# Optimization experiments

Measured on AMD Instinct MI355X. Metric: run time of the kernel, lower is better.

Reference implementation:

```python
import jax, jax.numpy as jnp
import numpy as np
import math

# ---- hyperparameters (from __init__) ----
S = 64.0
M = 0.45
EASY_MARGIN = False
ALPHA = 0.0
BETA = 0.0
EPS_OT = 0.1   # self.eps
NITER = 6      # self.niter
COS_M = math.cos(M)
SIN_M = math.sin(M)
TH = math.cos(math.pi - M)
MM = math.sin(math.pi - M) * M

# ---- shapes ----
B = 24
D_EMB = 512
N_CLASSES = 10000
C_CH = 256   # channels -> number of OT points per image
H = 14       # spatial -> point dim H*H = 196


def setup_inputs() -> dict:
    key = jax.random.key(0)
    k1, k2, k3, k4 = jax.random.split(key, 4)
    embeddings = jax.random.normal(k1, (B, D_EMB), dtype=jnp.float32)
    conv_features = jax.random.normal(k2, (B, C_CH, H, H), dtype=jnp.float32)
    label = jax.random.randint(k3, (B,), 0, 8)
    # nn.init.normal_(kernel, std=0.01)
    kernel = jax.random.normal(k4, (D_EMB, N_CLASSES), dtype=jnp.float32) * 0.01
    return {"embeddings": embeddings, "conv_features": conv_features,
            "kernel": kernel, "label": label, "epoch": 1}


def _cdist(x, y):
    # Euclidean pairwise distance via GEMM: x (n,d), y (m,d) -> (n,m)
    x2 = jnp.sum(x * x, axis=-1)[:, None]
    y2 = jnp.sum(y * y, axis=-1)[None, :]
    d2 = jnp.maximum(x2 + y2 - 2.0 * (x @ y.T), 0.0)
    return jnp.sqrt(d2 + 1e-12)


def _sinkhorn_dist(x, y):
    # Entropic OT distance <T, C> with uniform marginals, log-domain Sinkhorn.
    C = _cdist(x, y)                       # (n, m)
    n, m = C.shape
    log_mu = -jnp.log(jnp.float32(n))
    log_nu = -jnp.log(jnp.float32(m))
    f = jnp.zeros((n,), C.dtype)
    g = jnp.zeros((m,), C.dtype)
    for _ in range(NITER):  # fixed 6 iterations
        f = -EPS_OT * jax.nn.logsumexp((g[None, :] - C) / EPS_OT + log_nu, axis=1)
        g = -EPS_OT * jax.nn.logsumexp((f[:, None] - C) / EPS_OT + log_mu, axis=0)
    T = jnp.exp((f[:, None] + g[None, :] - C) / EPS_OT + log_mu + log_nu)
    return jnp.sum(T * C)


def reference(embeddings, conv_features, kernel, label, epoch):
    b = embeddings.shape[0]
    emb = embeddings / jnp.linalg.norm(embeddings, axis=1, keepdims=True)
    kn = kernel / jnp.linalg.norm(kernel, axis=0, keepdims=True)
    cos_theta = jnp.clip(emb @ kn, -1.0, 1.0)          # (B, n_classes)
    origin_cos = cos_theta

    rows = jnp.arange(b)
    tl = cos_theta[rows, label]                         # target logit (B,)
    sin_t = jnp.sqrt(jnp.maximum(1.0 - tl * tl, 0.0))
    ctm = tl * COS_M - sin_t * SIN_M
    if EASY_MARGIN:
        ftl = jnp.where(tl > 0.0, ctm, tl)
    else:
        ftl = jnp.where(tl > TH, ctm, tl - MM)
    cos_theta = cos_theta.at[rows, label].set(ftl)
    arcfaceloss = cos_theta * S

    # ---- triplet mining on embedding cosine similarities ----
    dists = emb @ emb.T                                 # (B, B) cosine sims
    eq = label[:, None] == label[None, :]               # (B, B) same-class mask
    # diff_low[a,p,n] = cos(a,n) - cos(a,p)
    diff = dists[:, None, :] - dists[:, :, None]        # (a, p, n)
    valid = eq[:, :, None] & (~eq)[:, None, :] & (diff > -ALPHA)
    n_cosine_pair = jnp.sum(valid)

    if epoch >= 0:
        feats = conv_features.reshape(b, conv_features.shape[1], -1)  # (B, C, H*H)
        # batched Sinkhorn distance for all (a,b) image pairs: (B, B)
        D = jax.vmap(lambda xa: jax.vmap(lambda xb: _sinkhorn_dist(xa, xb))(feats))(feats)
        dis = jnp.maximum(D[:, :, None] - D[:, None, :], -BETA)       # (a, p, n)
        hit = valid & (dis > 0.0)
        ot_pair = jnp.sum(hit)
        wass = jnp.sum(jnp.where(hit, dis, 0.0))
        wass_loss = jnp.where(wass > 0.0,
                              wass / jnp.maximum(ot_pair, 1).astype(wass.dtype),
                              jnp.zeros((), wass.dtype))
    else:
        ot_pair = jnp.zeros((), jnp.int32)
        wass_loss = jnp.zeros(())

    return (arcfaceloss, wass_loss, origin_cos * S, n_cosine_pair, ot_pair)
```

## Files before the change

kernel.cpp:

```cpp
#include <hip/hip_runtime.h>
#include <math.h>

#define B_SZ 24
#define D_EMBD 512
#define N_CLS 10000
#define CC 256
#define HH 196

#define S_SCALE 64.0f
#define COS_M 0.9004471023526769f
#define SIN_M 0.43496553411123023f
#define TH_C (-0.9004471023526769f)
#define MM_C 0.19573449035005357f
#define KSC 14.4269504088896f
#define C2E 0.0693147180559945f

typedef short bfrag8 __attribute__((ext_vector_type(8)));
typedef float facc4 __attribute__((ext_vector_type(4)));

#if __has_builtin(__builtin_amdgcn_exp2f)
#define EXP2F(x) __builtin_amdgcn_exp2f(x)
#else
#define EXP2F(x) exp2f(x)
#endif
#if __has_builtin(__builtin_amdgcn_logf)
#define LOG2F(x) __builtin_amdgcn_logf(x)
#else
#define LOG2F(x) __log2f(x)
#endif

__device__ inline unsigned short f2bf_rne(float x) {
    union { float f; unsigned u; } cv; cv.f = x;
    unsigned r = cv.u + 0x7FFFu + ((cv.u >> 16) & 1u);
    return (unsigned short)(r >> 16);
}
__device__ inline float bf2f(unsigned short h) {
    union { unsigned u; float f; } cv; cv.u = ((unsigned)h) << 16; return cv.f;
}

__global__ __launch_bounds__(1024) void k_pairs_all(const float* __restrict__ emb,
        const float* __restrict__ conv, float* __restrict__ dists,
        float* __restrict__ Dmat) {
    const int t = threadIdx.x;
    const int bid = blockIdx.x;

    if (bid >= 276) {
        int l = t & 63, w16 = t >> 6;
        if (bid == 276 && t < B_SZ) Dmat[t * B_SZ + t] = 0.f;
        int pid = (bid - 276) * 16 + w16;
        if (pid >= B_SZ * B_SZ) return;
        int i = pid / B_SZ, j = pid - (pid / B_SZ) * B_SZ;
        float sij = 0.f, sii = 0.f, sjj = 0.f;
        #pragma unroll
        for (int u = 0; u < 8; ++u) {
            float vi = emb[i*D_EMBD + u*64 + l];
            float vj = emb[j*D_EMBD + u*64 + l];
            sij = fmaf(vi, vj, sij); sii = fmaf(vi, vi, sii); sjj = fmaf(vj, vj, sjj);
        }
        #pragma unroll
        for (int o = 1; o < 64; o <<= 1) {
            sij += __shfl_xor(sij, o, 64);
            sii += __shfl_xor(sii, o, 64);
            sjj += __shfl_xor(sjj, o, 64);
        }
        if (l == 0) dists[pid] = sij * rsqrtf(sii * sjj);
        return;
    }

    __shared__ __align__(16) char smem[65536];
    unsigned short* Ah = (unsigned short*)smem;
    unsigned short* Al = Ah + 8192;
    unsigned short* Bh = Al + 8192;
    unsigned short* Bl = Bh + 8192;
    float* rowred = (float*)smem;
    float* colred = rowred + 1024;
    float* rm_l   = colred + 1024;
    float* z_l    = rm_l + 256;
    float* g_l    = z_l + 256;
    float* na_s   = g_l + 256;
    float* nb_s   = na_s + 256;
    float* wredF  = nb_s + 256;
    float* wredG  = wredF + 4;
    float* wredD  = wredG + 4;

    const int w = t >> 6;
    const int wr = w >> 2, wc = w & 3;
    const int q = (t >> 4) & 3, c0 = t & 15;
    const int R0 = wr * 64, C0 = wc * 64;

    int rem = bid, a = 0;
    while (rem >= 23 - a) { rem -= 23 - a; ++a; }
    int b = a + 1 + rem;
    const float* xa = conv + a*CC*HH;
    const float* xb = conv + b*CC*HH;

    const int sn = t >> 2;
    const int sch = t & 3;

    facc4 acc[4][4];
    #pragma unroll
    for (int i = 0; i < 4; ++i)
        #pragma unroll
        for (int j = 0; j < 4; ++j) acc[i][j] = (facc4){0.f, 0.f, 0.f, 0.f};

    float pa = 0.f, pb = 0.f;

    for (int ks = 0; ks < 224; ks += 32) {
        __syncthreads();
        #pragma unroll
        for (int p = 0; p < 2; ++p) {
            int k0 = ks + sch*8;
            const float* src = (p ? xb : xa) + sn*HH + k0;
            float v[8];
            if (k0 + 8 <= HH) {
                const float4* s4 = (const float4*)src;
                float4 u0 = s4[0], u1 = s4[1];
                v[0]=u0.x; v[1]=u0.y; v[2]=u0.z; v[3]=u0.w;
                v[4]=u1.x; v[5]=u1.y; v[6]=u1.z; v[7]=u1.w;
            } else {
                #pragma unroll
                for (int j = 0; j < 8; ++j) v[j] = (k0 + j < HH) ? src[j] : 0.f;
            }
            float ps = 0.f;
            union { unsigned short s[8]; bfrag8 v8; } uh, ul;
            #pragma unroll
            for (int j = 0; j < 8; ++j) {
                ps = fmaf(v[j], v[j], ps);
                unsigned short hb = f2bf_rne(v[j]);
                uh.s[j] = hb;
                ul.s[j] = f2bf_rne(v[j] - bf2f(hb));
            }
            if (p) pb += ps; else pa += ps;
            unsigned short* dh = (p ? Bh : Ah) + sn*32 + sch*8;
            unsigned short* dl = (p ? Bl : Al) + sn*32 + sch*8;
            *(bfrag8*)dh = uh.v8;
            *(bfrag8*)dl = ul.v8;
        }
        __syncthreads();
        bfrag8 bh4[4], bl4[4];
        #pragma unroll
        for (int tj = 0; tj < 4; ++tj) {
            int col = C0 + tj*16 + c0;
            bh4[tj] = *(const bfrag8*)(Bh + col*32 + q*8);
            bl4[tj] = *(const bfrag8*)(Bl + col*32 + q*8);
        }
        #pragma unroll
        for (int ti = 0; ti < 4; ++ti) {
            int row = R0 + ti*16 + c0;
            bfrag8 ah = *(const bfrag8*)(Ah + row*32 + q*8);
            bfrag8 al = *(const bfrag8*)(Al + row*32 + q*8);
            #pragma unroll
            for (int tj = 0; tj < 4; ++tj) {
                acc[ti][tj] = __builtin_amdgcn_mfma_f32_16x16x32_bf16(ah, bh4[tj], acc[ti][tj], 0, 0, 0);
                acc[ti][tj] = __builtin_amdgcn_mfma_f32_16x16x32_bf16(ah, bl4[tj], acc[ti][tj], 0, 0, 0);
                acc[ti][tj] = __builtin_amdgcn_mfma_f32_16x16x32_bf16(al, bh4[tj], acc[ti][tj], 0, 0, 0);
            }
        }
    }
    __syncthreads();

    pa += __shfl_xor(pa, 1, 64); pa += __shfl_xor(pa, 2, 64);
    pb += __shfl_xor(pb, 1, 64); pb += __shfl_xor(pb, 2, 64);
    if (sch == 0) { na_s[sn] = pa; nb_s[sn] = pb; }
    if (t < 256) g_l[t] = 0.f;
    if (t < 4) wredG[t] = 0.f;
    __syncthreads();

    facc4 E[4][4];
    {
        float nbv[4];
        #pragma unroll
        for (int tj = 0; tj < 4; ++tj) nbv[tj] = nb_s[C0 + tj*16 + c0];
        #pragma unroll
        for (int ti = 0; ti < 4; ++ti) {
            facc4 nav = *(const facc4*)&na_s[R0 + ti*16 + q*4];
            #pragma unroll
            for (int tj = 0; tj < 4; ++tj) {
                #pragma unroll
                for (int r = 0; r < 4; ++r) {
                    float d2 = fmaxf(nav[r] + nbv[tj] - 2.f*acc[ti][tj][r], 0.f);
                    E[ti][tj][r] = KSC * sqrtf(d2 + 1e-12f);
                }
            }
        }
    }

    const int istar = ((c0&1)<<3) | ((c0&2)<<1) | ((c0&4)>>1) | ((c0&8)>>3);
    const int rowstar = R0 + (istar>>2)*16 + q*4 + (istar&3);
    const int tjstar = ((q&1)<<1) | (q>>1);
    const int colstar = C0 + tjstar*16 + c0;

    {
        float v16[16];
        #pragma unroll
        for (int ti = 0; ti < 4; ++ti)
            #pragma unroll
            for (int r = 0; r < 4; ++r)
                v16[ti*4+r] = fminf(fminf(E[ti][0][r], E[ti][1][r]),
                                    fminf(E[ti][2][r], E[ti][3][r]));
        #pragma unroll
        for (int p = 0; p < 4; ++p) {
            const int m = 1 << p, hsz = 8 >> p;
            const bool hi = (c0 >> p) & 1;
            #pragma unroll
            for (int j = 0; j < hsz; ++j) {
                float mine = hi ? v16[j+hsz] : v16[j];
                float send = hi ? v16[j] : v16[j+hsz];
                v16[j] = fminf(mine, __shfl_xor(send, m, 64));
            }
        }
        rowred[wc*256 + rowstar] = v16[0];
    }
    __syncthreads();
    if (t < 256)
        rm_l[t] = fminf(fminf(rowred[t], rowred[256+t]), fminf(rowred[512+t], rowred[768+t]));
    __syncthreads();

    #pragma unroll
    for (int ti = 0; ti < 4; ++ti) {
        facc4 rmv = *(const facc4*)&rm_l[R0 + ti*16 + q*4];
        #pragma unroll
        for (int tj = 0; tj < 4; ++tj)
            #pragma unroll
            for (int r = 0; r < 4; ++r)
                E[ti][tj][r] = EXP2F(rmv[r] - E[ti][tj][r]);
    }

    #pragma unroll 1
    for (int it = 0; it < 6; ++it) {
        float Gmax = fmaxf(fmaxf(wredG[0], wredG[1]), fmaxf(wredG[2], wredG[3]));
        float P4[4];
        #pragma unroll
        for (int tj = 0; tj < 4; ++tj) P4[tj] = EXP2F(g_l[C0 + tj*16 + c0] - Gmax);
        float v16[16];
        #pragma unroll
        for (int ti = 0; ti < 4; ++ti)
            #pragma unroll
            for (int r = 0; r < 4; ++r) {
                float s = 0.f;
                #pragma unroll
                for (int tj = 0; tj < 4; ++tj) s = fmaf(E[ti][tj][r], P4[tj], s);
                v16[ti*4+r] = s;
            }
        #pragma unroll
        for (int p = 0; p < 4; ++p) {
            const int m = 1 << p, hsz = 8 >> p;
            const bool hi = (c0 >> p) & 1;
            #pragma unroll
            for (int j = 0; j < hsz; ++j) {
                float mine = hi ? v16[j+hsz] : v16[j];
                float send = hi ? v16[j] : v16[j+hsz];
                v16[j] = mine + __shfl_xor(send, m, 64);
            }
        }
        rowred[wc*256 + rowstar] = v16[0];
        __syncthreads();
        if (t < 256) {
            float s = rowred[t] + rowred[256+t] + rowred[512+t] + rowred[768+t];
            float z = 8.f - Gmax - LOG2F(s);
            z_l[t] = z;
            float m = z;
            #pragma unroll
            for (int o = 1; o < 64; o <<= 1) m = fmaxf(m, __shfl_xor(m, o, 64));
            if ((t & 63) == 0) wredF[t >> 6] = m;
        }
        __syncthreads();
        float M = fmaxf(fmaxf(wredF[0], wredF[1]), fmaxf(wredF[2], wredF[3]));
        float Q[16];
        #pragma unroll
        for (int ti = 0; ti < 4; ++ti) {
            facc4 zv = *(const facc4*)&z_l[R0 + ti*16 + q*4];
            #pragma unroll
            for (int r = 0; r < 4; ++r) Q[ti*4+r] = EXP2F(zv[r] - M);
        }
        float w4[4];
        #pragma unroll
        for (int tj = 0; tj < 4; ++tj) {
            float s = 0.f;
            #pragma unroll
            for (int ti = 0; ti < 4; ++ti)
                #pragma unroll
                for (int r = 0; r < 4; ++r) s = fmaf(E[ti][tj][r], Q[ti*4+r], s);
            w4[tj] = s;
        }
        #pragma unroll
        for (int p = 0; p < 2; ++p) {
            const int m = 16 << p, hsz = 2 >> p;
            const bool hi = (q >> p) & 1;
            #pragma unroll
            for (int j = 0; j < hsz; ++j) {
                float mine = hi ? w4[j+hsz] : w4[j];
                float send = hi ? w4[j] : w4[j+hsz];
                w4[j] = mine + __shfl_xor(send, m, 64);
            }
        }
        colred[wr*256 + colstar] = w4[0];
        __syncthreads();
        if (t < 256) {
            float s = colred[t] + colred[256+t] + colred[512+t] + colred[768+t];
            float G = 8.f - M - LOG2F(s);
            g_l[t] = G;
            float m = G;
            #pragma unroll
            for (int o = 1; o < 64; o <<= 1) m = fmaxf(m, __shfl_xor(m, o, 64));
            if ((t & 63) == 0) wredG[t >> 6] = m;
        }
        __syncthreads();
    }

    {
        float G4[4];
        #pragma unroll
        for (int tj = 0; tj < 4; ++tj) G4[tj] = g_l[C0 + tj*16 + c0] - 16.f;
        float d = 0.f;
        #pragma unroll
        for (int ti = 0; ti < 4; ++ti) {
            facc4 zv = *(const facc4*)&z_l[R0 + ti*16 + q*4];
            facc4 rmv = *(const facc4*)&rm_l[R0 + ti*16 + q*4];
            #pragma unroll
            for (int tj = 0; tj < 4; ++tj) {
                #pragma unroll
                for (int r = 0; r < 4; ++r) {
                    float e = fmaxf(E[ti][tj][r], 1e-45f);
                    float lE = LOG2F(e);
                    float ce = rmv[r] - lE;
                    d = fmaf(EXP2F(zv[r] + G4[tj] + lE), ce, d);
                }
            }
        }
        d *= C2E;
        #pragma unroll
        for (int o = 1; o < 64; o <<= 1) d += __shfl_xor(d, o, 64);
        if ((t & 63) == 0) wredD[w] = d;
        __syncthreads();
        if (t == 0) {
            float s = 0.f;
            #pragma unroll
            for (int i = 0; i < 16; ++i) s += wredD[i];
            Dmat[a*B_SZ + b] = s;
            Dmat[b*B_SZ + a] = s;
        }
    }
}

__global__ __launch_bounds__(256) void k_arc_fin(const float* __restrict__ emb,
        const float* __restrict__ kern, const int* __restrict__ label,
        const float* __restrict__ dists, const float* __restrict__ Dmat,
        float* __restrict__ out) {
    const int t = threadIdx.x;
    const int bid = blockIdx.x;

    if (bid == 313) {
        __shared__ float ds[576], Dm[576];
        __shared__ int lab[B_SZ];
        __shared__ float wls[4]; __shared__ int wnp[4], wot[4];
        for (int i = t; i < 576; i += 256) { ds[i] = dists[i]; Dm[i] = Dmat[i]; }
        if (t < B_SZ) lab[t] = label[t];
        __syncthreads();
        int np = 0, ot = 0; float wsum = 0.f;
        for (int idx = t; idx < 24*24*24; idx += 256) {
            int a2 = idx / 576;
            int rest = idx - a2*576;
            int p2 = rest / 24;
            int n2 = rest - p2*24;
            int la = lab[a2];
            if (la == lab[p2] && la != lab[n2]) {
                float diff = ds[a2*24 + n2] - ds[a2*24 + p2];
                if (diff > 0.f) {
                    ++np;
                    float dd = Dm[a2*24 + p2] - Dm[a2*24 + n2];
                    if (dd > 0.f) { ++ot; wsum += dd; }
                }
            }
        }
        #pragma unroll
        for (int o = 1; o < 64; o <<= 1) {
            np += __shfl_xor(np, o, 64);
            ot += __shfl_xor(ot, o, 64);
            wsum += __shfl_xor(wsum, o, 64);
        }
        int w = t >> 6;
        if ((t & 63) == 0) { wnp[w] = np; wot[w] = ot; wls[w] = wsum; }
        __syncthreads();
        if (t == 0) {
            int tnp = wnp[0]+wnp[1]+wnp[2]+wnp[3];
            int tot = wot[0]+wot[1]+wot[2]+wot[3];
            float tws = wls[0]+wls[1]+wls[2]+wls[3];
            int den = tot > 1 ? tot : 1;
            float wl = (tws > 0.f) ? tws / (float)den : 0.f;
            out[240000] = wl;
            out[480001] = (float)tnp;
// ... 39 lines not shown
    for (int u = 0; u < 16; ++u) {
        int kb = k0 + u*4;
        float kv0 = kern[(kb+0)*N_CLS + cL];
        float kv1 = kern[(kb+1)*N_CLS + cL];
        float kv2 = kern[(kb+2)*N_CLS + cL];
        float kv3 = kern[(kb+3)*N_CLS + cL];
        cn = fmaf(kv0,kv0,cn); cn = fmaf(kv1,kv1,cn);
        cn = fmaf(kv2,kv2,cn); cn = fmaf(kv3,kv3,cn);
        #pragma unroll
        for (int r = 0; r < B_SZ; ++r) {
            const float4 e = *(const float4*)&es[r*D_EMBD + kb];
            acc[r] = fmaf(e.x, kv0, acc[r]);
            acc[r] = fmaf(e.y, kv1, acc[r]);
            acc[r] = fmaf(e.z, kv2, acc[r]);
            acc[r] = fmaf(e.w, kv3, acc[r]);
        }
    }
    __syncthreads();
    #pragma unroll
    for (int r = 0; r < B_SZ; ++r) part[kc*800 + cc*25 + r] = acc[r];
    part[kc*800 + cc*25 + 24] = cn;
    __syncthreads();
    for (int j = t; j < 800; j += 256) {
        float s = 0.f;
        #pragma unroll
        for (int kk = 0; kk < 8; ++kk) s += part[kk*800 + j];
        resb[j] = s;
    }
    __syncthreads();
    for (int o = t; o < 768; o += 256) {
        int r = o >> 5, c2 = o & 31;
        int col = bid*32 + c2;
        if (col >= N_CLS) continue;
        float dot = resb[c2*25 + r];
        float invk = rsqrtf(resb[c2*25 + 24]);
        float cosv = fminf(fmaxf(dot * inv_s[r] * invk, -1.f), 1.f);
        float oc = cosv * S_SCALE;
        float af = oc;
        if (lab_s[r] == col) {
            float tl = cosv;
            float sint = sqrtf(fmaxf(1.f - tl*tl, 0.f));
            float ctm = tl*COS_M - sint*SIN_M;
            float ftl = (tl > TH_C) ? ctm : (tl - MM_C);
            af = ftl * S_SCALE;
        }
        out[r*N_CLS + col] = af;
        out[240001 + r*N_CLS + col] = oc;
    }
}

extern "C" void kernel_launch(void* const* d_in, const int* in_sizes, int n_in,
                              void* d_out, int out_size, void* d_ws, size_t ws_size,
                              hipStream_t stream) {
    (void)in_sizes; (void)n_in; (void)out_size; (void)ws_size;
    const float* emb  = (const float*)d_in[0];
    const float* conv = (const float*)d_in[1];
    const float* kern = (const float*)d_in[2];
    const int*   lab  = (const int*)d_in[3];
    float* out = (float*)d_out;
    float* ws  = (float*)d_ws;
    float* dists = ws;
    float* Dmat  = ws + 576;

    k_pairs_all<<<312, 1024, 0, stream>>>(emb, conv, dists, Dmat);
    k_arc_fin<<<314, 256, 0, stream>>>(emb, kern, lab, dists, Dmat, out);
}
```

Before: 204.1 us.

## Split OT pairs into GEMM+exp kernel and register-resident Sinkhorn kernel

Replaces the single fused per-pair kernel with two stages. The first stage uses 624 half-pair blocks of 512 threads that run the split-bf16 MFMA cost GEMM, compute row minima and write the exponentiated kernel matrix as bf16 to workspace. The second stage uses one 512-thread block per pair, holds that bf16 matrix in registers and runs the 6 Sinkhorn iterations plus the final cost sum. The goal is more parallelism and occupancy per stage. In exchange it adds about 36 MB of workspace traffic and an extra launch, keeps the old path as a fallback when workspace is too small, and relies on bf16 E values whose precision may differ.

```diff
diff --git a/kernel.cpp b/kernel.cpp
--- a/kernel.cpp
+++ b/kernel.cpp
@@ -36,6 +36,396 @@
 }
 __device__ inline float bf2f(unsigned short h) {
     union { unsigned u; float f; } cv; cv.u = ((unsigned)h) << 16; return cv.f;
+}
+__device__ inline float bflo(unsigned u) {
+    union { unsigned x; float f; } c; c.x = u << 16; return c.f;
+}
+__device__ inline float bfhi(unsigned u) {
+    union { unsigned x; float f; } c; c.x = u & 0xffff0000u; return c.f;
+}
+
+__global__ __launch_bounds__(512, 2) void k_gemmE(const float* __restrict__ emb,
+        const float* __restrict__ conv, float* __restrict__ dists,
+        float* __restrict__ Dmat, float* __restrict__ rm_ws,
+        unsigned short* __restrict__ E16) {
+    const int t = threadIdx.x;
+    const int bid = blockIdx.x;
+
+    if (bid >= 552) {
+        int l = t & 63, w16 = t >> 6;
+        if (bid == 552 && t < B_SZ) Dmat[t * B_SZ + t] = 0.f;
+        int pid = (bid - 552) * 8 + w16;
+        if (pid >= B_SZ * B_SZ) return;
+        int i = pid / B_SZ, j = pid - (pid / B_SZ) * B_SZ;
+        float sij = 0.f, sii = 0.f, sjj = 0.f;
+        #pragma unroll
+        for (int u = 0; u < 8; ++u) {
+            float vi = emb[i*D_EMBD + u*64 + l];
+            float vj = emb[j*D_EMBD + u*64 + l];
+            sij = fmaf(vi, vj, sij); sii = fmaf(vi, vi, sii); sjj = fmaf(vj, vj, sjj);
+        }
+        #pragma unroll
+        for (int o = 1; o < 64; o <<= 1) {
+            sij += __shfl_xor(sij, o, 64);
+            sii += __shfl_xor(sii, o, 64);
+            sjj += __shfl_xor(sjj, o, 64);
+        }
+        if (l == 0) dists[pid] = sij * rsqrtf(sii * sjj);
+        return;
+    }
+
+    __shared__ __align__(16) unsigned short AhS[128*32];
+    __shared__ __align__(16) unsigned short AlS[128*32];
+    __shared__ __align__(16) unsigned short BhS[256*32];
+    __shared__ __align__(16) unsigned short BlS[256*32];
+    __shared__ float na_s[128], nb_s[256];
+    __shared__ float rowred[4*128];
+    __shared__ float rm_l[128];
+
+    const int pair = bid >> 1, half = bid & 1;
+    int rem = pair, a = 0;
+    while (rem >= 23 - a) { rem -= 23 - a; ++a; }
+    int b = a + 1 + rem;
+    const float* xa = conv + a*CC*HH + half*128*HH;
+    const float* xb = conv + b*CC*HH;
+
+    const int w = t >> 6;
+    const int wrg = w >> 2, wcg = w & 3;
+    const int q = (t >> 4) & 3, c0 = t & 15;
+    const int R0l = wrg * 64, C0 = wcg * 64;
+
+    const int snA = t >> 2, schA = t & 3;
+    const int snB = t >> 1, khB = t & 1;
+
+    facc4 acc[4][4];
+    #pragma unroll
+    for (int i = 0; i < 4; ++i)
+        #pragma unroll
+        for (int j = 0; j < 4; ++j) acc[i][j] = (facc4){0.f, 0.f, 0.f, 0.f};
+
+    float pa = 0.f, pb = 0.f;
+
+    for (int ks = 0; ks < 224; ks += 32) {
+        __syncthreads();
+        {
+            int k0 = ks + schA*8;
+            const float* src = xa + snA*HH + k0;
+            float v[8];
+            if (k0 + 8 <= HH) {
+                const float4* s4 = (const float4*)src;
+                float4 u0 = s4[0], u1 = s4[1];
+                v[0]=u0.x; v[1]=u0.y; v[2]=u0.z; v[3]=u0.w;
+                v[4]=u1.x; v[5]=u1.y; v[6]=u1.z; v[7]=u1.w;
+            } else {
+                #pragma unroll
+                for (int j = 0; j < 8; ++j) v[j] = (k0 + j < HH) ? src[j] : 0.f;
+            }
+            float ps = 0.f;
+            union { unsigned short s[8]; bfrag8 v8; } uh, ul;
+            #pragma unroll
+            for (int j = 0; j < 8; ++j) {
+                ps = fmaf(v[j], v[j], ps);
+                unsigned short hb = f2bf_rne(v[j]);
+                uh.s[j] = hb;
+                ul.s[j] = f2bf_rne(v[j] - bf2f(hb));
+            }
+            pa += ps;
+            *(bfrag8*)&AhS[snA*32 + schA*8] = uh.v8;
+            *(bfrag8*)&AlS[snA*32 + schA*8] = ul.v8;
+        }
+        {
+            int k0 = ks + khB*16;
+            const float* src = xb + snB*HH + k0;
+            float v[16];
+            if (k0 + 16 <= HH) {
+                const float4* s4 = (const float4*)src;
+                #pragma unroll
+                for (int p4 = 0; p4 < 4; ++p4) {
+                    float4 u = s4[p4];
+                    v[p4*4+0]=u.x; v[p4*4+1]=u.y; v[p4*4+2]=u.z; v[p4*4+3]=u.w;
+                }
+            } else {
+                #pragma unroll
+                for (int j = 0; j < 16; ++j) v[j] = (k0 + j < HH) ? src[j] : 0.f;
+            }
+            float ps = 0.f;
+            union { unsigned short s[16]; bfrag8 v8[2]; } uh, ul;
+            #pragma unroll
+            for (int j = 0; j < 16; ++j) {
+                ps = fmaf(v[j], v[j], ps);
+                unsigned short hb = f2bf_rne(v[j]);
+                uh.s[j] = hb;
+                ul.s[j] = f2bf_rne(v[j] - bf2f(hb));
+            }
+            pb += ps;
+            *(bfrag8*)&BhS[snB*32 + khB*16] = uh.v8[0];
+            *(bfrag8*)&BhS[snB*32 + khB*16 + 8] = uh.v8[1];
+            *(bfrag8*)&BlS[snB*32 + khB*16] = ul.v8[0];
+            *(bfrag8*)&BlS[snB*32 + khB*16 + 8] = ul.v8[1];
+        }
+        __syncthreads();
+        bfrag8 bh4[4], bl4[4];
+        #pragma unroll
+        for (int tj = 0; tj < 4; ++tj) {
+            int col = C0 + tj*16 + c0;
+            bh4[tj] = *(const bfrag8*)&BhS[col*32 + q*8];
+            bl4[tj] = *(const bfrag8*)&BlS[col*32 + q*8];
+        }
+        #pragma unroll
+        for (int ti = 0; ti < 4; ++ti) {
+            int row = R0l + ti*16 + c0;
+            bfrag8 ah = *(const bfrag8*)&AhS[row*32 + q*8];
+            bfrag8 al = *(const bfrag8*)&AlS[row*32 + q*8];
+            #pragma unroll
+            for (int tj = 0; tj < 4; ++tj) {
+                acc[ti][tj] = __builtin_amdgcn_mfma_f32_16x16x32_bf16(ah, bh4[tj], acc[ti][tj], 0, 0, 0);
+                acc[ti][tj] = __builtin_amdgcn_mfma_f32_16x16x32_bf16(ah, bl4[tj], acc[ti][tj], 0, 0, 0);
+                acc[ti][tj] = __builtin_amdgcn_mfma_f32_16x16x32_bf16(al, bh4[tj], acc[ti][tj], 0, 0, 0);
+            }
+        }
+    }
+
+    pa += __shfl_xor(pa, 1, 64); pa += __shfl_xor(pa, 2, 64);
+    pb += __shfl_xor(pb, 1, 64);
+    if (schA == 0) na_s[snA] = pa;
+    if (khB == 0) nb_s[snB] = pb;
+    __syncthreads();
+
+    facc4 Cv[4][4];
+    {
+        float nbv[4];
+        #pragma unroll
+        for (int tj = 0; tj < 4; ++tj) nbv[tj] = nb_s[C0 + tj*16 + c0];
+        #pragma unroll
+        for (int ti = 0; ti < 4; ++ti) {
+            facc4 nav = *(const facc4*)&na_s[R0l + ti*16 + q*4];
+            #pragma unroll
+            for (int tj = 0; tj < 4; ++tj) {
+                #pragma unroll
+                for (int r = 0; r < 4; ++r) {
+                    float d2 = fmaxf(nav[r] + nbv[tj] - 2.f*acc[ti][tj][r], 0.f);
+                    Cv[ti][tj][r] = KSC * sqrtf(d2 + 1e-12f);
+                }
+            }
+        }
+    }
+
+    const int istar = ((c0&1)<<3) | ((c0&2)<<1) | ((c0&4)>>1) | ((c0&8)>>3);
+    const int rowstar = R0l + (istar>>2)*16 + q*4 + (istar&3);
+
+    {
+        float v16[16];
+        #pragma unroll
+        for (int ti = 0; ti < 4; ++ti)
+            #pragma unroll
+            for (int r = 0; r < 4; ++r)
+                v16[ti*4+r] = fminf(fminf(Cv[ti][0][r], Cv[ti][1][r]),
+                                    fminf(Cv[ti][2][r], Cv[ti][3][r]));
+        #pragma unroll
+        for (int p = 0; p < 4; ++p) {
+            const int m = 1 << p, hsz = 8 >> p;
+            const bool hi = (c0 >> p) & 1;
+            #pragma unroll
+            for (int j = 0; j < hsz; ++j) {
+                float mine = hi ? v16[j+hsz] : v16[j];
+                float send = hi ? v16[j] : v16[j+hsz];
+                v16[j] = fminf(mine, __shfl_xor(send, m, 64));
+            }
+        }
+        rowred[wcg*128 + rowstar] = v16[0];
+    }
+    __syncthreads();
+    if (t < 128) {
+        float m = fminf(fminf(rowred[t], rowred[128+t]), fminf(rowred[256+t], rowred[384+t]));
+        rm_l[t] = m;
+        rm_ws[pair*256 + half*128 + t] = m;
+    }
+    __syncthreads();
+
+    {
+        const int s = ((half*2 + wrg)*2 + (wcg>>1))*64 + q*16 + c0;
+        unsigned short* Ep = E16 + (size_t)pair*65536 + s*128;
+        #pragma unroll
+        for (int ti = 0; ti < 4; ++ti) {
+            facc4 rmv = *(const facc4*)&rm_l[R0l + ti*16 + q*4];
+            #pragma unroll
+            for (int tj = 0; tj < 4; ++tj) {
+                float e0 = EXP2F(rmv[0] - Cv[ti][tj][0]);
+                float e1 = EXP2F(rmv[1] - Cv[ti][tj][1]);
+                float e2 = EXP2F(rmv[2] - Cv[ti][tj][2]);
+                float e3 = EXP2F(rmv[3] - Cv[ti][tj][3]);
+                unsigned lo = (unsigned)f2bf_rne(e0) | ((unsigned)f2bf_rne(e1) << 16);
+                unsigned hi = (unsigned)f2bf_rne(e2) | ((unsigned)f2bf_rne(e3) << 16);
+                uint2 pk; pk.x = lo; pk.y = hi;
+                int j0 = ti*32 + ((wcg&1)*4 + tj)*4;
+                *(uint2*)&Ep[j0] = pk;
+            }
+        }
+    }
+}
+
+__global__ __launch_bounds__(512, 4) void k_sink(const unsigned short* __restrict__ E16,
+        const float* __restrict__ rm_ws, float* __restrict__ Dmat) {
+    __shared__ float rowred[2*256];
+    __shared__ float colred[4*256];
+    __shared__ float z_l[256], g_l[256], rm_l[256];
+    __shared__ float wredF[4], wredG[4], wredD[8];
+
+    const int t = threadIdx.x;
+    const int w = t >> 6;
+    const int wr = w >> 1, wc = w & 1;
+    const int q = (t >> 4) & 3, c0 = t & 15;
+    const int R0 = wr * 64, C0 = wc * 128;
+    const int pair = blockIdx.x;
+
+    int rem = pair, a = 0;
+    while (rem >= 23 - a) { rem -= 23 - a; ++a; }
+    int b = a + 1 + rem;
+
+    unsigned ue[64];
+    {
+        const uint4* eb = (const uint4*)(E16 + (size_t)pair*65536 + t*128);
+        #pragma unroll
+        for (int i = 0; i < 16; ++i) {
+            uint4 v = eb[i];
+            ue[i*4+0] = v.x; ue[i*4+1] = v.y; ue[i*4+2] = v.z; ue[i*4+3] = v.w;
+        }
+    }
+    if (t < 256) { rm_l[t] = rm_ws[pair*256 + t]; g_l[t] = 0.f; }
+    if (t < 4) wredG[t] = 0.f;
+    __syncthreads();
+
+    const int istar = ((c0&1)<<3) | ((c0&2)<<1) | ((c0&4)>>1) | ((c0&8)>>3);
+    const int rowstar = R0 + (istar>>2)*16 + q*4 + (istar&3);
+
+    #pragma unroll 1
+    for (int it = 0; it < 6; ++it) {
+        float Gmax = fmaxf(fmaxf(wredG[0], wredG[1]), fmaxf(wredG[2], wredG[3]));
+        float P8[8];
+        #pragma unroll
+        for (int tj = 0; tj < 8; ++tj) P8[tj] = EXP2F(g_l[C0 + tj*16 + c0] - Gmax);
+        float v16[16];
+        #pragma unroll
+        for (int ti = 0; ti < 4; ++ti) {
+            float s0 = 0.f, s1 = 0.f, s2 = 0.f, s3 = 0.f;
+            #pragma unroll
+            for (int tj = 0; tj < 8; ++tj) {
+                unsigned u0 = ue[(ti*8+tj)*2], u1 = ue[(ti*8+tj)*2+1];
+                float p = P8[tj];
+                s0 = fmaf(bflo(u0), p, s0); s1 = fmaf(bfhi(u0), p, s1);
+                s2 = fmaf(bflo(u1), p, s2); s3 = fmaf(bfhi(u1), p, s3);
+            }
+            v16[ti*4+0]=s0; v16[ti*4+1]=s1; v16[ti*4+2]=s2; v16[ti*4+3]=s3;
+        }
+        #pragma unroll
+        for (int p = 0; p < 4; ++p) {
+            const int m = 1 << p, hsz = 8 >> p;
+            const bool hi = (c0 >> p) & 1;
+            #pragma unroll
+            for (int j = 0; j < hsz; ++j) {
+                float mine = hi ? v16[j+hsz] : v16[j];
+                float send = hi ? v16[j] : v16[j+hsz];
+                v16[j] = mine + __shfl_xor(send, m, 64);
+            }
+        }
+        rowred[wc*256 + rowstar] = v16[0];
+        __syncthreads();
+        if (t < 256) {
+            float s = rowred[t] + rowred[256+t];
+            float z = 8.f - Gmax - LOG2F(s);
+            z_l[t] = z;
+            float m = z;
+            #pragma unroll
+            for (int o = 1; o < 64; o <<= 1) m = fmaxf(m, __shfl_xor(m, o, 64));
+            if ((t & 63) == 0) wredF[t >> 6] = m;
+        }
+        __syncthreads();
+        float M = fmaxf(fmaxf(wredF[0], wredF[1]), fmaxf(wredF[2], wredF[3]));
+        float Q[16];
+        #pragma unroll
+        for (int ti = 0; ti < 4; ++ti) {
+            facc4 zv = *(const facc4*)&z_l[R0 + ti*16 + q*4];
+            #pragma unroll
+            for (int r = 0; r < 4; ++r) Q[ti*4+r] = EXP2F(zv[r] - M);
+        }
+        float w8[8];
+        #pragma unroll
+        for (int tj = 0; tj < 8; ++tj) {
+            float s = 0.f;
+            #pragma unroll
+            for (int ti = 0; ti < 4; ++ti) {
+                unsigned u0 = ue[(ti*8+tj)*2], u1 = ue[(ti*8+tj)*2+1];
+                s = fmaf(bflo(u0), Q[ti*4+0], s); s = fmaf(bfhi(u0), Q[ti*4+1], s);
+                s = fmaf(bflo(u1), Q[ti*4+2], s); s = fmaf(bfhi(u1), Q[ti*4+3], s);
+            }
+            w8[tj] = s;
+        }
+        {
+            #pragma unroll
+            for (int p = 0; p < 2; ++p) {
+                const int m = 16 << p, hsz = 4 >> p;
+                const bool hi = p == 0 ? (q & 1) : ((q >> 1) & 1);
+                #pragma unroll
+                for (int j = 0; j < hsz; ++j) {
+                    float mine = hi ? w8[j+hsz] : w8[j];
+                    float send = hi ? w8[j] : w8[j+hsz];
+                    w8[j] = mine + __shfl_xor(send, m, 64);
+                }
+            }
+            int tjb = (q&1)*4 + (q>>1)*2;
+            colred[wr*256 + C0 + (tjb+0)*16 + c0] = w8[0];
+            colred[wr*256 + C0 + (tjb+1)*16 + c0] = w8[1];
+        }
+        __syncthreads();
+        if (t < 256) {
+            float s = colred[t] + colred[256+t] + colred[512+t] + colred[768+t];
+            float G = 8.f - M - LOG2F(s);
+            g_l[t] = G;
+            float m = G;
+            #pragma unroll
+            for (int o = 1; o < 64; o <<= 1) m = fmaxf(m, __shfl_xor(m, o, 64));
+            if ((t & 63) == 0) wredG[t >> 6] = m;
+        }
+        __syncthreads();
+    }
+
+    {
+        float G8[8];
+        #pragma unroll
+        for (int tj = 0; tj < 8; ++tj) G8[tj] = g_l[C0 + tj*16 + c0] - 16.f;
+        float d = 0.f;
+        #pragma unroll
+        for (int ti = 0; ti < 4; ++ti) {
+            facc4 zv = *(const facc4*)&z_l[R0 + ti*16 + q*4];
+            facc4 rmv = *(const facc4*)&rm_l[R0 + ti*16 + q*4];
+            #pragma unroll
+            for (int tj = 0; tj < 8; ++tj) {
+                unsigned u0 = ue[(ti*8+tj)*2], u1 = ue[(ti*8+tj)*2+1];
+                float gb = G8[tj];
+                float e, lE;
+                e = fmaxf(bflo(u0), 1e-38f); lE = LOG2F(e);
+                d = fmaf(EXP2F(zv[0] + gb + lE), rmv[0] - lE, d);
+                e = fmaxf(bfhi(u0), 1e-38f); lE = LOG2F(e);
+                d = fmaf(EXP2F(zv[1] + gb + lE), rmv[1] - lE, d);
+                e = fmaxf(bflo(u1), 1e-38f); lE = LOG2F(e);
+                d = fmaf(EXP2F(zv[2] + gb + lE), rmv[2] - lE, d);
+                e = fmaxf(bfhi(u1), 1e-38f); lE = LOG2F(e);
+                d = fmaf(EXP2F(zv[3] + gb + lE), rmv[3] - lE, d);
+            }
+        }
+        d *= C2E;
+        #pragma unroll
+        for (int o = 1; o < 64; o <<= 1) d += __shfl_xor(d, o, 64);
+        if ((t & 63) == 0) wredD[w] = d;
+        __syncthreads();
+        if (t == 0) {
+            float s = 0.f;
+            #pragma unroll
+            for (int i = 0; i < 8; ++i) s += wredD[i];
+            Dmat[a*B_SZ + b] = s;
+            Dmat[b*B_SZ + a] = s;
+        }
+    }
 }
 
 __global__ __launch_bounds__(1024) void k_pairs_all(const float* __restrict__ emb,
@@ -323,8 +713,7 @@
                 for (int r = 0; r < 4; ++r) {
                     float e = fmaxf(E[ti][tj][r], 1e-45f);
                     float lE = LOG2F(e);
-                    float ce = rmv[r] - lE;
-                    d = fmaf(EXP2F(zv[r] + G4[tj] + lE), ce, d);
+                    d = fmaf(EXP2F(zv[r] + G4[tj] + lE), rmv[r] - lE, d);
                 }
             }
         }
@@ -482,7 +871,7 @@
 extern "C" void kernel_launch(void* const* d_in, const int* in_sizes, int n_in,
                               void* d_out, int out_size, void* d_ws, size_t ws_size,
                               hipStream_t stream) {
-    (void)in_sizes; (void)n_in; (void)out_size; (void)ws_size;
+    (void)in_sizes; (void)n_in; (void)out_size;
     const float* emb  = (const float*)d_in[0];
     const float* conv = (const float*)d_in[1];
     const float* kern = (const float*)d_in[2];
@@ -491,7 +880,15 @@
     float* ws  = (float*)d_ws;
     float* dists = ws;
     float* Dmat  = ws + 576;
-
-    k_pairs_all<<<312, 1024, 0, stream>>>(emb, conv, dists, Dmat);
+    float* rm_ws = ws + 1152;
+    unsigned short* E16 = (unsigned short*)(ws + 71808);
+
+    const size_t ws_needed = (size_t)71808*4 + (size_t)276*65536*2;
+    if (ws_size >= ws_needed) {
+        k_gemmE<<<624, 512, 0, stream>>>(emb, conv, dists, Dmat, rm_ws, E16);
+        k_sink<<<276, 512, 0, stream>>>(E16, rm_ws, Dmat);
+    } else {
+        k_pairs_all<<<312, 1024, 0, stream>>>(emb, conv, dists, Dmat);
+    }
     k_arc_fin<<<314, 256, 0, stream>>>(emb, kern, lab, dists, Dmat, out);
 }
```

After: 281.0 us. 37.7% more time.

## Halve Sinkhorn block to 512 threads, store kernel matrix packed as bf16 in registers

Applied to the files above, without the earlier changes.

The pairwise Sinkhorn kernel now runs with 512 threads per block and computes the 256x256 cost matrix in four 128x128 quadrants. The exponentiated kernel matrix is kept in registers packed as bf16 pairs instead of fp32, and quadrant row minima are merged afterwards with a rescale. The aim is to cut LDS use and register pressure so more blocks fit per CU, and to shrink the per-thread kernel matrix footprint. In exchange it adds more sync rounds and GEMM staging passes, and bf16 storage of the kernel matrix loses precision in the Sinkhorn iterations.

```diff
diff --git a/kernel.cpp b/kernel.cpp
--- a/kernel.cpp
+++ b/kernel.cpp
@@ -37,8 +37,17 @@
 __device__ inline float bf2f(unsigned short h) {
     union { unsigned u; float f; } cv; cv.u = ((unsigned)h) << 16; return cv.f;
 }
-
-__global__ __launch_bounds__(1024) void k_pairs_all(const float* __restrict__ emb,
+__device__ inline float bflo(unsigned u) {
+    union { unsigned x; float f; } c; c.x = u << 16; return c.f;
+}
+__device__ inline float bfhi(unsigned u) {
+    union { unsigned x; float f; } c; c.x = u & 0xffff0000u; return c.f;
+}
+__device__ inline unsigned packbf(float a, float b) {
+    return (unsigned)f2bf_rne(a) | ((unsigned)f2bf_rne(b) << 16);
+}
+
+__global__ __launch_bounds__(512, 4) void k_pairs2(const float* __restrict__ emb,
         const float* __restrict__ conv, float* __restrict__ dists,
         float* __restrict__ Dmat) {
     const int t = threadIdx.x;
@@ -47,7 +56,7 @@
     if (bid >= 276) {
         int l = t & 63, w16 = t >> 6;
         if (bid == 276 && t < B_SZ) Dmat[t * B_SZ + t] = 0.f;
-        int pid = (bid - 276) * 16 + w16;
+        int pid = (bid - 276) * 8 + w16;
         if (pid >= B_SZ * B_SZ) return;
         int i = pid / B_SZ, j = pid - (pid / B_SZ) * B_SZ;
         float sij = 0.f, sii = 0.f, sjj = 0.f;
@@ -67,26 +76,25 @@
         return;
     }
 
-    __shared__ __align__(16) char smem[65536];
-    unsigned short* Ah = (unsigned short*)smem;
-    unsigned short* Al = Ah + 8192;
-    unsigned short* Bh = Al + 8192;
-    unsigned short* Bl = Bh + 8192;
-    float* rowred = (float*)smem;
-    float* colred = rowred + 1024;
-    float* rm_l   = colred + 1024;
-    float* z_l    = rm_l + 256;
-    float* g_l    = z_l + 256;
-    float* na_s   = g_l + 256;
-    float* nb_s   = na_s + 256;
-    float* wredF  = nb_s + 256;
-    float* wredG  = wredF + 4;
-    float* wredD  = wredG + 4;
+    __shared__ __align__(16) unsigned short AhS[128*32];
+    __shared__ __align__(16) unsigned short AlS[128*32];
+    __shared__ __align__(16) unsigned short BhS[128*32];
+    __shared__ __align__(16) unsigned short BlS[128*32];
+    __shared__ __align__(16) float na_s[256];
+    __shared__ float nb_s[256];
+    __shared__ float rowred[1024];
+    __shared__ __align__(16) float rmq[512];
+    __shared__ __align__(16) float rm_l[256];
+    __shared__ __align__(16) float z_l[256];
+    __shared__ float g_l[256];
+    __shared__ float colred[512];
+    __shared__ float wredF[4], wredG[4], wredD[8];
 
     const int w = t >> 6;
-    const int wr = w >> 2, wc = w & 3;
+    const int wr2 = w >> 2;
+    const int wc2 = w & 3;
     const int q = (t >> 4) & 3, c0 = t & 15;
-    const int R0 = wr * 64, C0 = wc * 64;
+    const int sn = t >> 2, sch = t & 3;
 
     int rem = bid, a = 0;
     while (rem >= 23 - a) { rem -= 23 - a; ++a; }
@@ -94,136 +102,167 @@
     const float* xa = conv + a*CC*HH;
     const float* xb = conv + b*CC*HH;
 
-    const int sn = t >> 2;
-    const int sch = t & 3;
-
-    facc4 acc[4][4];
+    unsigned ue[64];
+
+    const int istar = ((c0&1)<<3) | ((c0&2)<<1) | ((c0&4)>>1) | ((c0&8)>>3);
+    const int rloc_star = wr2*64 + (istar>>2)*16 + q*4 + (istar&3);
+
     #pragma unroll
-    for (int i = 0; i < 4; ++i)
-        #pragma unroll
-        for (int j = 0; j < 4; ++j) acc[i][j] = (facc4){0.f, 0.f, 0.f, 0.f};
-
-    float pa = 0.f, pb = 0.f;
-
-    for (int ks = 0; ks < 224; ks += 32) {
-        __syncthreads();
-        #pragma unroll
-        for (int p = 0; p < 2; ++p) {
-            int k0 = ks + sch*8;
-            const float* src = (p ? xb : xa) + sn*HH + k0;
-            float v[8];
-            if (k0 + 8 <= HH) {
-                const float4* s4 = (const float4*)src;
-                float4 u0 = s4[0], u1 = s4[1];
-                v[0]=u0.x; v[1]=u0.y; v[2]=u0.z; v[3]=u0.w;
-                v[4]=u1.x; v[5]=u1.y; v[6]=u1.z; v[7]=u1.w;
-            } else {
-                #pragma unroll
-                for (int j = 0; j < 8; ++j) v[j] = (k0 + j < HH) ? src[j] : 0.f;
-            }
-            float ps = 0.f;
-            union { unsigned short s[8]; bfrag8 v8; } uh, ul;
-            #pragma unroll
-            for (int j = 0; j < 8; ++j) {
-                ps = fmaf(v[j], v[j], ps);
-                unsigned short hb = f2bf_rne(v[j]);
-                uh.s[j] = hb;
-                ul.s[j] = f2bf_rne(v[j] - bf2f(hb));
-            }
-            if (p) pb += ps; else pa += ps;
-            unsigned short* dh = (p ? Bh : Ah) + sn*32 + sch*8;
-            unsigned short* dl = (p ? Bl : Al) + sn*32 + sch*8;
-            *(bfrag8*)dh = uh.v8;
-            *(bfrag8*)dl = ul.v8;
-        }
-        __syncthreads();
-        bfrag8 bh4[4], bl4[4];
-        #pragma unroll
-        for (int tj = 0; tj < 4; ++tj) {
-            int col = C0 + tj*16 + c0;
-            bh4[tj] = *(const bfrag8*)(Bh + col*32 + q*8);
-            bl4[tj] = *(const bfrag8*)(Bl + col*32 + q*8);
-        }
+    for (int qq = 0; qq < 4; ++qq) {
+        const int rh = qq >> 1, ch = qq & 1;
+        const float* xA = xa + rh*128*HH;
+        const float* xB = xb + ch*128*HH;
+        facc4 acc[4][2];
+        #pragma unroll
+        for (int i = 0; i < 4; ++i) { acc[i][0] = (facc4){0,0,0,0}; acc[i][1] = (facc4){0,0,0,0}; }
+        float pqa = 0.f, pqb = 0.f;
+
+        #pragma unroll 1
+        for (int ks = 0; ks < 224; ks += 32) {
+            __syncthreads();
+            const int k0 = ks + sch*8;
+            #pragma unroll
+            for (int p = 0; p < 2; ++p) {
+                const float* src = (p ? xB : xA) + sn*HH + k0;
+                float v[8];
+                if (k0 + 8 <= HH) {
+                    const float4* s4 = (const float4*)src;
+                    float4 u0 = s4[0], u1 = s4[1];
+                    v[0]=u0.x; v[1]=u0.y; v[2]=u0.z; v[3]=u0.w;
+                    v[4]=u1.x; v[5]=u1.y; v[6]=u1.z; v[7]=u1.w;
+                } else {
+                    #pragma unroll
+                    for (int j = 0; j < 8; ++j) v[j] = (k0 + j < HH) ? src[j] : 0.f;
+                }
+                float ps = 0.f;
+                union { unsigned short s[8]; bfrag8 v8; } uh, ul;
+                #pragma unroll
+                for (int j = 0; j < 8; ++j) {
+                    ps = fmaf(v[j], v[j], ps);
+                    unsigned short hb = f2bf_rne(v[j]);
+                    uh.s[j] = hb;
+                    ul.s[j] = f2bf_rne(v[j] - bf2f(hb));
+                }
+                if (p) { if (rh == 0) pqb += ps; }
+                else   { if (ch == 0) pqa += ps; }
+                *(bfrag8*)&((p ? BhS : AhS)[sn*32 + sch*8]) = uh.v8;
+                *(bfrag8*)&((p ? BlS : AlS)[sn*32 + sch*8]) = ul.v8;
+            }
+            __syncthreads();
+            bfrag8 bh2[2], bl2[2];
+            #pragma unroll
+            for (int tj = 0; tj < 2; ++tj) {
+                int col = wc2*32 + tj*16 + c0;
+                bh2[tj] = *(const bfrag8*)&BhS[col*32 + q*8];
+                bl2[tj] = *(const bfrag8*)&BlS[col*32 + q*8];
+            }
+            #pragma unroll
+            for (int ti = 0; ti < 4; ++ti) {
+                int row = wr2*64 + ti*16 + c0;
+                bfrag8 ah = *(const bfrag8*)&AhS[row*32 + q*8];
+                bfrag8 al = *(const bfrag8*)&AlS[row*32 + q*8];
+                #pragma unroll
+                for (int tj = 0; tj < 2; ++tj) {
+                    acc[ti][tj] = __builtin_amdgcn_mfma_f32_16x16x32_bf16(ah, bh2[tj], acc[ti][tj], 0, 0, 0);
+                    acc[ti][tj] = __builtin_amdgcn_mfma_f32_16x16x32_bf16(ah, bl2[tj], acc[ti][tj], 0, 0, 0);
+                    acc[ti][tj] = __builtin_amdgcn_mfma_f32_16x16x32_bf16(al, bh2[tj], acc[ti][tj], 0, 0, 0);
+                }
+            }
+        }
+        if (ch == 0) {
+            pqa += __shfl_xor(pqa, 1, 64); pqa += __shfl_xor(pqa, 2, 64);
+            if (sch == 0) na_s[rh*128 + sn] = pqa;
+        }
+        if (rh == 0) {
+            pqb += __shfl_xor(pqb, 1, 64); pqb += __shfl_xor(pqb, 2, 64);
+            if (sch == 0) nb_s[ch*128 + sn] = pqb;
+        }
+        __syncthreads();
+
+        facc4 Cv[4][2];
+        {
+            float nbv[2];
+            #pragma unroll
+            for (int tj = 0; tj < 2; ++tj) nbv[tj] = nb_s[ch*128 + wc2*32 + tj*16 + c0];
+            #pragma unroll
+            for (int ti = 0; ti < 4; ++ti) {
+                facc4 nav = *(const facc4*)&na_s[rh*128 + wr2*64 + ti*16 + q*4];
+                #pragma unroll
+                for (int tj = 0; tj < 2; ++tj) {
+                    #pragma unroll
+                    for (int r = 0; r < 4; ++r) {
+                        float d2 = fmaxf(nav[r] + nbv[tj] - 2.f*acc[ti][tj][r], 0.f);
+                        Cv[ti][tj][r] = KSC * sqrtf(d2 + 1e-12f);
+                    }
+                }
+            }
+        }
+        {
+            float v16[16];
+            #pragma unroll
+            for (int ti = 0; ti < 4; ++ti)
+                #pragma unroll
+                for (int r = 0; r < 4; ++r)
+                    v16[ti*4+r] = fminf(Cv[ti][0][r], Cv[ti][1][r]);
+            #pragma unroll
+            for (int p = 0; p < 4; ++p) {
+                const int m = 1 << p, hsz = 8 >> p;
+                const bool hi = (c0 >> p) & 1;
+                #pragma unroll
+                for (int j = 0; j < hsz; ++j) {
+                    float mine = hi ? v16[j+hsz] : v16[j];
+                    float send = hi ? v16[j] : v16[j+hsz];
+                    v16[j] = fminf(mine, __shfl_xor(send, m, 64));
+                }
+            }
+            rowred[wc2*128 + rloc_star] = v16[0];
+        }
+        __syncthreads();
+        if (t < 128) {
+            float m = fminf(fminf(rowred[t], rowred[128+t]), fminf(rowred[256+t], rowred[384+t]));
+            rmq[ch*256 + rh*128 + t] = m;
+        }
+        __syncthreads();
         #pragma unroll
         for (int ti = 0; ti < 4; ++ti) {
-            int row = R0 + ti*16 + c0;
-            bfrag8 ah = *(const bfrag8*)(Ah + row*32 + q*8);
-            bfrag8 al = *(const bfrag8*)(Al + row*32 + q*8);
-            #pragma unroll
-            for (int tj = 0; tj < 4; ++tj) {
-                acc[ti][tj] = __builtin_amdgcn_mfma_f32_16x16x32_bf16(ah, bh4[tj], acc[ti][tj], 0, 0, 0);
-                acc[ti][tj] = __builtin_amdgcn_mfma_f32_16x16x32_bf16(ah, bl4[tj], acc[ti][tj], 0, 0, 0);
-                acc[ti][tj] = __builtin_amdgcn_mfma_f32_16x16x32_bf16(al, bh4[tj], acc[ti][tj], 0, 0, 0);
-            }
-        }
-    }
-    __syncthreads();
-
-    pa += __shfl_xor(pa, 1, 64); pa += __shfl_xor(pa, 2, 64);
-    pb += __shfl_xor(pb, 1, 64); pb += __shfl_xor(pb, 2, 64);
-    if (sch == 0) { na_s[sn] = pa; nb_s[sn] = pb; }
-    if (t < 256) g_l[t] = 0.f;
+            facc4 rmv = *(const facc4*)&rmq[ch*256 + rh*128 + wr2*64 + ti*16 + q*4];
+            #pragma unroll
+            for (int tj = 0; tj < 2; ++tj) {
+                float e0 = EXP2F(rmv[0] - Cv[ti][tj][0]);
+                float e1 = EXP2F(rmv[1] - Cv[ti][tj][1]);
+                float e2 = EXP2F(rmv[2] - Cv[ti][tj][2]);
+                float e3 = EXP2F(rmv[3] - Cv[ti][tj][3]);
+                ue[qq*16 + ti*4 + tj*2 + 0] = packbf(e0, e1);
+                ue[qq*16 + ti*4 + tj*2 + 1] = packbf(e2, e3);
+            }
+        }
+    }
+
+    if (t < 256) { rm_l[t] = fminf(rmq[t], rmq[256+t]); g_l[t] = 0.f; }
     if (t < 4) wredG[t] = 0.f;
     __syncthreads();
-
-    facc4 E[4][4];
-    {
-        float nbv[4];
-        #pragma unroll
-        for (int tj = 0; tj < 4; ++tj) nbv[tj] = nb_s[C0 + tj*16 + c0];
+    #pragma unroll
+    for (int rh = 0; rh < 2; ++rh) {
         #pragma unroll
         for (int ti = 0; ti < 4; ++ti) {
-            facc4 nav = *(const facc4*)&na_s[R0 + ti*16 + q*4];
-            #pragma unroll
-            for (int tj = 0; tj < 4; ++tj) {
-                #pragma unroll
-                for (int r = 0; r < 4; ++r) {
-                    float d2 = fmaxf(nav[r] + nbv[tj] - 2.f*acc[ti][tj][r], 0.f);
-                    E[ti][tj][r] = KSC * sqrtf(d2 + 1e-12f);
-                }
-            }
-        }
-    }
-
-    const int istar = ((c0&1)<<3) | ((c0&2)<<1) | ((c0&4)>>1) | ((c0&8)>>3);
-    const int rowstar = R0 + (istar>>2)*16 + q*4 + (istar&3);
-    const int tjstar = ((q&1)<<1) | (q>>1);
-    const int colstar = C0 + tjstar*16 + c0;
-
-    {
-        float v16[16];
-        #pragma unroll
-        for (int ti = 0; ti < 4; ++ti)
-            #pragma unroll
-            for (int r = 0; r < 4; ++r)
-                v16[ti*4+r] = fminf(fminf(E[ti][0][r], E[ti][1][r]),
-                                    fminf(E[ti][2][r], E[ti][3][r]));
-        #pragma unroll
-        for (int p = 0; p < 4; ++p) {
-            const int m = 1 << p, hsz = 8 >> p;
-            const bool hi = (c0 >> p) & 1;
-            #pragma unroll
-            for (int j = 0; j < hsz; ++j) {
-                float mine = hi ? v16[j+hsz] : v16[j];
-                float send = hi ? v16[j] : v16[j+hsz];
-                v16[j] = fminf(mine, __shfl_xor(send, m, 64));
-            }
-        }
-        rowred[wc*256 + rowstar] = v16[0];
-    }
-    __syncthreads();
-    if (t < 256)
-        rm_l[t] = fminf(fminf(rowred[t], rowred[256+t]), fminf(rowred[512+t], rowred[768+t]));
-    __syncthreads();
-
-    #pragma unroll
-    for (int ti = 0; ti < 4; ++ti) {
-        facc4 rmv = *(const facc4*)&rm_l[R0 + ti*16 + q*4];
-        #pragma unroll
-        for (int tj = 0; tj < 4; ++tj)
-            #pragma unroll
-            for (int r = 0; r < 4; ++r)
-                E[ti][tj][r] = EXP2F(rmv[r] - E[ti][tj][r]);
+            const int rb = rh*128 + wr2*64 + ti*16 + q*4;
+            facc4 rmv = *(const facc4*)&rm_l[rb];
+            #pragma unroll
+            for (int ch = 0; ch < 2; ++ch) {
+                facc4 rq = *(const facc4*)&rmq[ch*256 + rb];
+                float s0 = EXP2F(rmv[0] - rq[0]);
+                float s1 = EXP2F(rmv[1] - rq[1]);
+                float s2 = EXP2F(rmv[2] - rq[2]);
+                float s3 = EXP2F(rmv[3] - rq[3]);
+                #pragma unroll
+                for (int tj = 0; tj < 2; ++tj) {
+                    const int i0 = (rh*2+ch)*16 + ti*4 + tj*2;
+                    unsigned u0 = ue[i0], u1 = ue[i0+1];
+                    ue[i0]   = packbf(bflo(u0)*s0, bfhi(u0)*s1);
+                    ue[i0+1] = packbf(bflo(u1)*s2, bfhi(u1)*s3);
+                }
+            }
+        }
     }
 
     #pragma unroll 1
@@ -231,29 +270,41 @@
         float Gmax = fmaxf(fmaxf(wredG[0], wredG[1]), fmaxf(wredG[2], wredG[3]));
         float P4[4];
         #pragma unroll
-        for (int tj = 0; tj < 4; ++tj) P4[tj] = EXP2F(g_l[C0 + tj*16 + c0] - Gmax);
-        float v16[16];
-        #pragma unroll
-        for (int ti = 0; ti < 4; ++ti)
-            #pragma unroll
-            for (int r = 0; r < 4; ++r) {
-                float s = 0.f;
-                #pragma unroll
-                for (int tj = 0; tj < 4; ++tj) s = fmaf(E[ti][tj][r], P4[tj], s);
-                v16[ti*4+r] = s;
-            }
-        #pragma unroll
-        for (int p = 0; p < 4; ++p) {
-            const int m = 1 << p, hsz = 8 >> p;
-            const bool hi = (c0 >> p) & 1;
-            #pragma unroll
-            for (int j = 0; j < hsz; ++j) {
-                float mine = hi ? v16[j+hsz] : v16[j];
-                float send = hi ? v16[j] : v16[j+hsz];
-                v16[j] = mine + __shfl_xor(send, m, 64);
-            }
-        }
-        rowred[wc*256 + rowstar] = v16[0];
+        for (int ch = 0; ch < 2; ++ch)
+            #pragma unroll
+            for (int tj = 0; tj < 2; ++tj)
+                P4[ch*2+tj] = EXP2F(g_l[ch*128 + wc2*32 + tj*16 + c0] - Gmax);
+        #pragma unroll
+        for (int rh = 0; rh < 2; ++rh) {
+            float v16[16];
+            #pragma unroll
+            for (int ti = 0; ti < 4; ++ti) {
+                float s0 = 0.f, s1 = 0.f, s2 = 0.f, s3 = 0.f;
+                #pragma unroll
+                for (int ch = 0; ch < 2; ++ch)
+                    #pragma unroll
+                    for (int tj = 0; tj < 2; ++tj) {
+                        const int i0 = (rh*2+ch)*16 + ti*4 + tj*2;
+                        unsigned u0 = ue[i0], u1 = ue[i0+1];
+                        float p = P4[ch*2+tj];
+                        s0 = fmaf(bflo(u0), p, s0); s1 = fmaf(bfhi(u0), p, s1);
+                        s2 = fmaf(bflo(u1), p, s2); s3 = fmaf(bfhi(u1), p, s3);
+                    }
+                v16[ti*4+0]=s0; v16[ti*4+1]=s1; v16[ti*4+2]=s2; v16[ti*4+3]=s3;
+            }
+            #pragma unroll
+            for (int p = 0; p < 4; ++p) {
+                const int m = 1 << p, hsz = 8 >> p;
+                const bool hi = (c0 >> p) & 1;
+                #pragma unroll
+                for (int j = 0; j < hsz; ++j) {
+                    float mine = hi ? v16[j+hsz] : v16[j];
+                    float send = hi ? v16[j] : v16[j+hsz];
+                    v16[j] = mine + __shfl_xor(send, m, 64);
+                }
+            }
+            rowred[wc2*256 + rh*128 + rloc_star] = v16[0];
+        }
         __syncthreads();
         if (t < 256) {
             float s = rowred[t] + rowred[256+t] + rowred[512+t] + rowred[768+t];
@@ -266,38 +317,44 @@
         }
         __syncthreads();
         float M = fmaxf(fmaxf(wredF[0], wredF[1]), fmaxf(wredF[2], wredF[3]));
-        float Q[16];
-        #pragma unroll
-        for (int ti = 0; ti < 4; ++ti) {
-            facc4 zv = *(const facc4*)&z_l[R0 + ti*16 + q*4];
-            #pragma unroll
-            for (int r = 0; r < 4; ++r) Q[ti*4+r] = EXP2F(zv[r] - M);
-        }
-        float w4[4];
-        #pragma unroll
-        for (int tj = 0; tj < 4; ++tj) {
-            float s = 0.f;
-            #pragma unroll
-            for (int ti = 0; ti < 4; ++ti)
-                #pragma unroll
-                for (int r = 0; r < 4; ++r) s = fmaf(E[ti][tj][r], Q[ti*4+r], s);
-            w4[tj] = s;
-        }
-        #pragma unroll
-        for (int p = 0; p < 2; ++p) {
-            const int m = 16 << p, hsz = 2 >> p;
-            const bool hi = (q >> p) & 1;
-            #pragma unroll
-            for (int j = 0; j < hsz; ++j) {
-                float mine = hi ? w4[j+hsz] : w4[j];
-                float send = hi ? w4[j] : w4[j+hsz];
-                w4[j] = mine + __shfl_xor(send, m, 64);
-            }
-        }
-        colred[wr*256 + colstar] = w4[0];
+        float w4[4] = {0.f, 0.f, 0.f, 0.f};
+        #pragma unroll
+        for (int rh = 0; rh < 2; ++rh)
+            #pragma unroll
+            for (int ti = 0; ti < 4; ++ti) {
+                facc4 zv = *(const facc4*)&z_l[rh*128 + wr2*64 + ti*16 + q*4];
+                float Q0 = EXP2F(zv[0] - M), Q1 = EXP2F(zv[1] - M);
+                float Q2 = EXP2F(zv[2] - M), Q3 = EXP2F(zv[3] - M);
+                #pragma unroll
+                for (int ch = 0; ch < 2; ++ch)
+                    #pragma unroll
+                    for (int tj = 0; tj < 2; ++tj) {
+                        const int i0 = (rh*2+ch)*16 + ti*4 + tj*2;
+                        unsigned u0 = ue[i0], u1 = ue[i0+1];
+                        float s = w4[ch*2+tj];
+                        s = fmaf(bflo(u0), Q0, s); s = fmaf(bfhi(u0), Q1, s);
+                        s = fmaf(bflo(u1), Q2, s); s = fmaf(bfhi(u1), Q3, s);
+                        w4[ch*2+tj] = s;
+                    }
+            }
+        {
+            #pragma unroll
+            for (int p = 0; p < 2; ++p) {
+                const int m = 16 << p, hsz = 2 >> p;
+                const bool hi = p == 0 ? (q & 1) : ((q >> 1) & 1);
+                #pragma unroll
+                for (int j = 0; j < hsz; ++j) {
+                    float mine = hi ? w4[j+hsz] : w4[j];
+                    float send = hi ? w4[j] : w4[j+hsz];
+                    w4[j] = mine + __shfl_xor(send, m, 64);
+                }
+            }
+            const int colstar = (q&1)*128 + wc2*32 + (q>>1)*16 + c0;
+            colred[wr2*256 + colstar] = w4[0];
+        }
         __syncthreads();
         if (t < 256) {
-            float s = colred[t] + colred[256+t] + colred[512+t] + colred[768+t];
+            float s = colred[t] + colred[256+t];
             float G = 8.f - M - LOG2F(s);
             g_l[t] = G;
             float m = G;
@@ -311,23 +368,36 @@
     {
         float G4[4];
         #pragma unroll
-        for (int tj = 0; tj < 4; ++tj) G4[tj] = g_l[C0 + tj*16 + c0] - 16.f;
+        for (int ch = 0; ch < 2; ++ch)
+            #pragma unroll
+            for (int tj = 0; tj < 2; ++tj)
+                G4[ch*2+tj] = g_l[ch*128 + wc2*32 + tj*16 + c0] - 16.f;
         float d = 0.f;
         #pragma unroll
-        for (int ti = 0; ti < 4; ++ti) {
-            facc4 zv = *(const facc4*)&z_l[R0 + ti*16 + q*4];
-            facc4 rmv = *(const facc4*)&rm_l[R0 + ti*16 + q*4];
-            #pragma unroll
-            for (int tj = 0; tj < 4; ++tj) {
-                #pragma unroll
-                for (int r = 0; r < 4; ++r) {
-                    float e = fmaxf(E[ti][tj][r], 1e-45f);
-                    float lE = LOG2F(e);
-                    float ce = rmv[r] - lE;
-                    d = fmaf(EXP2F(zv[r] + G4[tj] + lE), ce, d);
-                }
-            }
-        }
+        for (int rh = 0; rh < 2; ++rh)
+            #pragma unroll
+            for (int ti = 0; ti < 4; ++ti) {
+                const int rb = rh*128 + wr2*64 + ti*16 + q*4;
+                facc4 zv = *(const facc4*)&z_l[rb];
+                facc4 rmv = *(const facc4*)&rm_l[rb];
+                #pragma unroll
+                for (int ch = 0; ch < 2; ++ch)
+                    #pragma unroll
+                    for (int tj = 0; tj < 2; ++tj) {
+                        const int i0 = (rh*2+ch)*16 + ti*4 + tj*2;
+                        unsigned u0 = ue[i0], u1 = ue[i0+1];
+                        float gb = G4[ch*2+tj];
+                        float e, lE;
+                        e = fmaxf(bflo(u0), 1e-38f); lE = LOG2F(e);
+                        d = fmaf(EXP2F(zv[0] + gb + lE), rmv[0] - lE, d);
+                        e = fmaxf(bfhi(u0), 1e-38f); lE = LOG2F(e);
+                        d = fmaf(EXP2F(zv[1] + gb + lE), rmv[1] - lE, d);
+                        e = fmaxf(bflo(u1), 1e-38f); lE = LOG2F(e);
+                        d = fmaf(EXP2F(zv[2] + gb + lE), rmv[2] - lE, d);
+                        e = fmaxf(bfhi(u1), 1e-38f); lE = LOG2F(e);
+                        d = fmaf(EXP2F(zv[3] + gb + lE), rmv[3] - lE, d);
+                    }
+            }
         d *= C2E;
         #pragma unroll
         for (int o = 1; o < 64; o <<= 1) d += __shfl_xor(d, o, 64);
@@ -336,7 +406,7 @@
         if (t == 0) {
             float s = 0.f;
             #pragma unroll
-            for (int i = 0; i < 16; ++i) s += wredD[i];
+            for (int i = 0; i < 8; ++i) s += wredD[i];
             Dmat[a*B_SZ + b] = s;
             Dmat[b*B_SZ + a] = s;
         }
@@ -492,6 +562,6 @@
     float* dists = ws;
     float* Dmat  = ws + 576;
 
-    k_pairs_all<<<312, 1024, 0, stream>>>(emb, conv, dists, Dmat);
+    k_pairs2<<<348, 512, 0, stream>>>(emb, conv, dists, Dmat);
     k_arc_fin<<<314, 256, 0, stream>>>(emb, kern, lab, dists, Dmat, out);
 }
```

After: 328.3 us. +60.8%, slower.
